# Kernel tuning notes

Measured on AMD Instinct MI355X. Metric: run time of the kernel, lower is better.

## Reference

```python
import jax, jax.numpy as jnp
import numpy as np

# Coefficients of the 16 differentiable logic gates expressed over the basis
# [1, a, b, a*b]. Row i corresponds to gate i in the standard difflogic order:
# 0:0, 1:a&b, 2:a&~b, 3:a, 4:~a&b, 5:b, 6:xor, 7:or, 8:nor, 9:xnor,
# 10:~b, 11:b=>a, 12:~a, 13:a=>b, 14:nand, 15:1
GATE_COEFFS = np.array([
    [0, 0, 0, 0],
    [0, 0, 0, 1],
    [0, 1, 0, -1],
    [0, 1, 0, 0],
    [0, 0, 1, -1],
    [0, 0, 1, 0],
    [0, 1, 1, -2],
    [0, 1, 1, -1],
    [1, -1, -1, 1],
    [1, -1, -1, 2],
    [1, 0, -1, 0],
    [1, 0, -1, 1],
    [1, -1, 0, 0],
    [1, -1, 0, 1],
    [1, 0, 0, -1],
    [1, 0, 0, 0],
], dtype=np.float32)

IN_DIM = 8192
OUT_DIM = 8192
BATCH = 8192
TAU = 1.0


def setup_inputs() -> dict:
    key = jax.random.key(0)
    k1, k2, k3, k4 = jax.random.split(key, 4)
    x = jax.random.uniform(k1, (BATCH, IN_DIM), dtype=jnp.float32)
    weight = jax.random.normal(k2, (OUT_DIM, 16), dtype=jnp.float32)
    idx_a = jax.random.randint(k3, (OUT_DIM,), 0, IN_DIM, dtype=jnp.int64 if jax.config.jax_enable_x64 else jnp.int32)
    idx_b = jax.random.randint(k4, (OUT_DIM,), 0, IN_DIM, dtype=jnp.int64 if jax.config.jax_enable_x64 else jnp.int32)
    return {"x": x, "weight": weight, "idx_a": idx_a, "idx_b": idx_b}


def reference(x, weight, idx_a, idx_b):
    # Gather the two inputs of each neuron: [B, out_dim]
    a = x[:, idx_a]
    b = x[:, idx_b]
    # Soft gate mixture: softmax over 16 gates per neuron (training, 'soft')
    w = jax.nn.softmax(weight / TAU, axis=-1)  # [out_dim, 16]
    # Since every gate is affine in {1, a, b, ab}, collapse the 16-gate
    # weighted sum into per-neuron coefficients: c = w @ G  -> [out_dim, 4]
    c = w @ jnp.asarray(GATE_COEFFS)
    out = c[:, 0] + c[:, 1] * a + c[:, 2] * b + c[:, 3] * (a * b)
    return out
```

## Files before the change

kernel.cpp:

```cpp
#include <hip/hip_runtime.h>
#include <hip/hip_bf16.h>
#include <math.h>

#define IN_DIM  8192
#define OUT_DIM 8192
#define BATCH   8192

__device__ __constant__ float GC0[16] = {0,0,0,0, 0,0,0,0, 1,1,1,1, 1,1,1,1};
__device__ __constant__ float GC1[16] = {0,0,1,1, 0,0,1,1, -1,-1,0,0, -1,-1,0,0};
__device__ __constant__ float GC2[16] = {0,0,0,0, 1,1,1,1, -1,-1,-1,-1, 0,0,0,0};
__device__ __constant__ float GC3[16] = {0,1,-1,0, -1,0,-2,-1, 1,2,0,1, 0,1,-1,0};

__global__ __launch_bounds__(256) void compute_c_kernel(
    const float* __restrict__ weight, float4* __restrict__ c)
{
    int row = blockIdx.x * 256 + threadIdx.x;
    if (row >= OUT_DIM) return;
    const float* wr = weight + (size_t)row * 16;
    float v[16];
    float m = -1e30f;
#pragma unroll
    for (int i = 0; i < 16; ++i) { v[i] = wr[i]; m = fmaxf(m, v[i]); }
    float s = 0.f;
#pragma unroll
    for (int i = 0; i < 16; ++i) { v[i] = __expf(v[i] - m); s += v[i]; }
    float inv = 1.0f / s;
    float c0 = 0.f, c1 = 0.f, c2 = 0.f, c3 = 0.f;
#pragma unroll
    for (int i = 0; i < 16; ++i) {
        c0 = fmaf(v[i], GC0[i], c0);
        c1 = fmaf(v[i], GC1[i], c1);
        c2 = fmaf(v[i], GC2[i], c2);
        c3 = fmaf(v[i], GC3[i], c3);
    }
    c[row] = make_float4(c0 * inv, c1 * inv, c2 * inv, c3 * inv);
}

__global__ __launch_bounds__(256) void gate_main_kernel(
    const float* __restrict__ x,
    const float4* __restrict__ c,
    const int4* __restrict__ ia4,
    const int4* __restrict__ ib4,
    float4* __restrict__ out)
{
    __shared__ float xrow[IN_DIM];
    const int b = blockIdx.x;
    const float4* xr4 = (const float4*)(x + (size_t)b * IN_DIM);
    float4* xs4 = (float4*)xrow;
#pragma unroll
    for (int i = 0; i < IN_DIM / 4 / 256; ++i)
        xs4[i * 256 + threadIdx.x] = xr4[i * 256 + threadIdx.x];
    __syncthreads();

    float4* orow = out + (size_t)b * (OUT_DIM / 4);
#pragma unroll
    for (int it = 0; it < OUT_DIM / 4 / 256; ++it) {
        int j4 = it * 256 + threadIdx.x;
        int4 ia = ia4[j4];
        int4 ib = ib4[j4];
        float4 cA = c[4 * j4 + 0];
        float4 cB = c[4 * j4 + 1];
        float4 cC = c[4 * j4 + 2];
        float4 cD = c[4 * j4 + 3];

        float a0 = xrow[ia.x], b0 = xrow[ib.x];
        float a1 = xrow[ia.y], b1 = xrow[ib.y];
        float a2 = xrow[ia.z], b2 = xrow[ib.z];
        float a3 = xrow[ia.w], b3 = xrow[ib.w];

        float4 o;
        o.x = fmaf(a0, fmaf(b0, cA.w, cA.y), fmaf(b0, cA.z, cA.x));
        o.y = fmaf(a1, fmaf(b1, cB.w, cB.y), fmaf(b1, cB.z, cB.x));
        o.z = fmaf(a2, fmaf(b2, cC.w, cC.y), fmaf(b2, cC.z, cC.x));
        o.w = fmaf(a3, fmaf(b3, cD.w, cD.y), fmaf(b3, cD.z, cD.x));
        orow[j4] = o;
    }
}

extern "C" void kernel_launch(void* const* d_in, const int* in_sizes, int n_in,
                              void* d_out, int out_size, void* d_ws, size_t ws_size,
                              hipStream_t stream) {
    const float* x      = (const float*)d_in[0];
    const float* weight = (const float*)d_in[1];
    const int*   idx_a  = (const int*)d_in[2];
    const int*   idx_b  = (const int*)d_in[3];
    float* out = (float*)d_out;

    float4* c = (float4*)d_ws;

    compute_c_kernel<<<OUT_DIM / 256, 256, 0, stream>>>(weight, c);
    gate_main_kernel<<<BATCH, 256, 0, stream>>>(
        x, c, (const int4*)idx_a, (const int4*)idx_b, (float4*)out);
}
```

Measured before the change: 484.0 us.

## Process two batch rows per block with 1024 threads and nontemporal output stores

```diff
diff --git a/kernel.cpp b/kernel.cpp
--- a/kernel.cpp
+++ b/kernel.cpp
@@ -1,10 +1,13 @@
 #include <hip/hip_runtime.h>
-#include <hip/hip_bf16.h>
 #include <math.h>
 
 #define IN_DIM  8192
 #define OUT_DIM 8192
 #define BATCH   8192
+#define RPB     2
+#define T       1024
+
+typedef float f32x4 __attribute__((ext_vector_type(4)));
 
 __device__ __constant__ float GC0[16] = {0,0,0,0, 0,0,0,0, 1,1,1,1, 1,1,1,1};
 __device__ __constant__ float GC1[16] = {0,0,1,1, 0,0,1,1, -1,-1,0,0, -1,-1,0,0};
@@ -36,26 +39,31 @@
     c[row] = make_float4(c0 * inv, c1 * inv, c2 * inv, c3 * inv);
 }
 
-__global__ __launch_bounds__(256) void gate_main_kernel(
+__global__ __launch_bounds__(T, 8) void gate_main_kernel(
     const float* __restrict__ x,
     const float4* __restrict__ c,
     const int4* __restrict__ ia4,
     const int4* __restrict__ ib4,
-    float4* __restrict__ out)
+    float* __restrict__ out)
 {
-    __shared__ float xrow[IN_DIM];
-    const int b = blockIdx.x;
-    const float4* xr4 = (const float4*)(x + (size_t)b * IN_DIM);
-    float4* xs4 = (float4*)xrow;
+    __shared__ float4 xrow4[RPB * IN_DIM / 4];
+    float* xrow = (float*)xrow4;
+    const size_t b0 = (size_t)blockIdx.x * RPB;
+
+    const float4* xr4 = (const float4*)(x + b0 * IN_DIM);
 #pragma unroll
-    for (int i = 0; i < IN_DIM / 4 / 256; ++i)
-        xs4[i * 256 + threadIdx.x] = xr4[i * 256 + threadIdx.x];
+    for (int i = 0; i < (RPB * IN_DIM / 4) / T; ++i)
+        xrow4[i * T + threadIdx.x] = xr4[i * T + threadIdx.x];
     __syncthreads();
 
-    float4* orow = out + (size_t)b * (OUT_DIM / 4);
+    const float* x0 = xrow;
+    const float* x1 = xrow + IN_DIM;
+    f32x4* orow0 = (f32x4*)(out + b0 * OUT_DIM);
+    f32x4* orow1 = orow0 + (OUT_DIM / 4);
+
 #pragma unroll
-    for (int it = 0; it < OUT_DIM / 4 / 256; ++it) {
-        int j4 = it * 256 + threadIdx.x;
+    for (int it = 0; it < OUT_DIM / 4 / T; ++it) {
+        int j4 = it * T + threadIdx.x;
         int4 ia = ia4[j4];
         int4 ib = ib4[j4];
         float4 cA = c[4 * j4 + 0];
@@ -63,17 +71,30 @@
         float4 cC = c[4 * j4 + 2];
         float4 cD = c[4 * j4 + 3];
 
-        float a0 = xrow[ia.x], b0 = xrow[ib.x];
-        float a1 = xrow[ia.y], b1 = xrow[ib.y];
-        float a2 = xrow[ia.z], b2 = xrow[ib.z];
-        float a3 = xrow[ia.w], b3 = xrow[ib.w];
-
-        float4 o;
-        o.x = fmaf(a0, fmaf(b0, cA.w, cA.y), fmaf(b0, cA.z, cA.x));
-        o.y = fmaf(a1, fmaf(b1, cB.w, cB.y), fmaf(b1, cB.z, cB.x));
-        o.z = fmaf(a2, fmaf(b2, cC.w, cC.y), fmaf(b2, cC.z, cC.x));
-        o.w = fmaf(a3, fmaf(b3, cD.w, cD.y), fmaf(b3, cD.z, cD.x));
-        orow[j4] = o;
+        {
+            float a0 = x0[ia.x], v0 = x0[ib.x];
+            float a1 = x0[ia.y], v1 = x0[ib.y];
+            float a2 = x0[ia.z], v2 = x0[ib.z];
+            float a3 = x0[ia.w], v3 = x0[ib.w];
+            f32x4 o;
+            o.x = fmaf(a0, fmaf(v0, cA.w, cA.y), fmaf(v0, cA.z, cA.x));
+            o.y = fmaf(a1, fmaf(v1, cB.w, cB.y), fmaf(v1, cB.z, cB.x));
+            o.z = fmaf(a2, fmaf(v2, cC.w, cC.y), fmaf(v2, cC.z, cC.x));
+            o.w = fmaf(a3, fmaf(v3, cD.w, cD.y), fmaf(v3, cD.z, cD.x));
+            __builtin_nontemporal_store(o, &orow0[j4]);
+        }
+        {
+            float a0 = x1[ia.x], v0 = x1[ib.x];
+            float a1 = x1[ia.y], v1 = x1[ib.y];
+            float a2 = x1[ia.z], v2 = x1[ib.z];
+            float a3 = x1[ia.w], v3 = x1[ib.w];
+            f32x4 o;
+            o.x = fmaf(a0, fmaf(v0, cA.w, cA.y), fmaf(v0, cA.z, cA.x));
+            o.y = fmaf(a1, fmaf(v1, cB.w, cB.y), fmaf(v1, cB.z, cB.x));
+            o.z = fmaf(a2, fmaf(v2, cC.w, cC.y), fmaf(v2, cC.z, cC.x));
+            o.w = fmaf(a3, fmaf(v3, cD.w, cD.y), fmaf(v3, cD.z, cD.x));
+            __builtin_nontemporal_store(o, &orow1[j4]);
+        }
     }
 }
 
@@ -89,6 +110,6 @@
     float4* c = (float4*)d_ws;
 
     compute_c_kernel<<<OUT_DIM / 256, 256, 0, stream>>>(weight, c);
-    gate_main_kernel<<<BATCH, 256, 0, stream>>>(
-        x, c, (const int4*)idx_a, (const int4*)idx_b, (float4*)out);
+    gate_main_kernel<<<BATCH / RPB, T, 0, stream>>>(
+        x, c, (const int4*)idx_a, (const int4*)idx_b, out);
 }
```

After: 461.5 us. -4.7%, faster.

## Process 16 batch rows per block with register-cached coefficients and double-buffered prefetch

Applied to the files above, without the earlier changes.

```diff
diff --git a/kernel.cpp b/kernel.cpp
--- a/kernel.cpp
+++ b/kernel.cpp
@@ -1,10 +1,11 @@
 #include <hip/hip_runtime.h>
-#include <hip/hip_bf16.h>
 #include <math.h>
 
 #define IN_DIM  8192
 #define OUT_DIM 8192
 #define BATCH   8192
+#define ROWS    16
+#define T       1024
 
 __device__ __constant__ float GC0[16] = {0,0,0,0, 0,0,0,0, 1,1,1,1, 1,1,1,1};
 __device__ __constant__ float GC1[16] = {0,0,1,1, 0,0,1,1, -1,-1,0,0, -1,-1,0,0};
@@ -36,44 +37,74 @@
     c[row] = make_float4(c0 * inv, c1 * inv, c2 * inv, c3 * inv);
 }
 
-__global__ __launch_bounds__(256) void gate_main_kernel(
+__global__ __launch_bounds__(T, 4) void gate_main_kernel(
     const float* __restrict__ x,
     const float4* __restrict__ c,
     const int4* __restrict__ ia4,
     const int4* __restrict__ ib4,
     float4* __restrict__ out)
 {
-    __shared__ float xrow[IN_DIM];
-    const int b = blockIdx.x;
-    const float4* xr4 = (const float4*)(x + (size_t)b * IN_DIM);
-    float4* xs4 = (float4*)xrow;
-#pragma unroll
-    for (int i = 0; i < IN_DIM / 4 / 256; ++i)
-        xs4[i * 256 + threadIdx.x] = xr4[i * 256 + threadIdx.x];
+    __shared__ float buf[2][IN_DIM];
+    const int tid = threadIdx.x;
+    const size_t r0 = (size_t)blockIdx.x * ROWS;
+
+    const int q0 = tid, q1 = tid + T;
+    const int4 iaA = ia4[q0], ibA = ib4[q0];
+    const int4 iaB = ia4[q1], ibB = ib4[q1];
+    const float4 cA0 = c[4*q0+0], cA1 = c[4*q0+1], cA2 = c[4*q0+2], cA3 = c[4*q0+3];
+    const float4 cB0 = c[4*q1+0], cB1 = c[4*q1+1], cB2 = c[4*q1+2], cB3 = c[4*q1+3];
+
+    {
+        const float4* src4 = (const float4*)(x + r0 * IN_DIM);
+        float4* dst4 = (float4*)buf[0];
+        dst4[tid]     = src4[tid];
+        dst4[tid + T] = src4[tid + T];
+    }
     __syncthreads();
 
-    float4* orow = out + (size_t)b * (OUT_DIM / 4);
-#pragma unroll
-    for (int it = 0; it < OUT_DIM / 4 / 256; ++it) {
-        int j4 = it * 256 + threadIdx.x;
-        int4 ia = ia4[j4];
-        int4 ib = ib4[j4];
-        float4 cA = c[4 * j4 + 0];
-        float4 cB = c[4 * j4 + 1];
-        float4 cC = c[4 * j4 + 2];
-        float4 cD = c[4 * j4 + 3];
+    int cur = 0;
+    for (int r = 0; r < ROWS; ++r) {
+        float4 p0 = make_float4(0,0,0,0), p1 = make_float4(0,0,0,0);
+        if (r + 1 < ROWS) {
+            const float4* src4 = (const float4*)(x + (r0 + r + 1) * IN_DIM);
+            p0 = src4[tid];
+            p1 = src4[tid + T];
+        }
 
-        float a0 = xrow[ia.x], b0 = xrow[ib.x];
-        float a1 = xrow[ia.y], b1 = xrow[ib.y];
-        float a2 = xrow[ia.z], b2 = xrow[ib.z];
-        float a3 = xrow[ia.w], b3 = xrow[ib.w];
+        const float* xr = buf[cur];
+        float4* orow = out + (r0 + r) * (OUT_DIM / 4);
+        {
+            float a0 = xr[iaA.x], b0 = xr[ibA.x];
+            float a1 = xr[iaA.y], b1 = xr[ibA.y];
+            float a2 = xr[iaA.z], b2 = xr[ibA.z];
+            float a3 = xr[iaA.w], b3 = xr[ibA.w];
+            float4 o;
+            o.x = fmaf(a0, fmaf(b0, cA0.w, cA0.y), fmaf(b0, cA0.z, cA0.x));
+            o.y = fmaf(a1, fmaf(b1, cA1.w, cA1.y), fmaf(b1, cA1.z, cA1.x));
+            o.z = fmaf(a2, fmaf(b2, cA2.w, cA2.y), fmaf(b2, cA2.z, cA2.x));
+            o.w = fmaf(a3, fmaf(b3, cA3.w, cA3.y), fmaf(b3, cA3.z, cA3.x));
+            orow[q0] = o;
+        }
+        {
+            float a0 = xr[iaB.x], b0 = xr[ibB.x];
+            float a1 = xr[iaB.y], b1 = xr[ibB.y];
+            float a2 = xr[iaB.z], b2 = xr[ibB.z];
+            float a3 = xr[iaB.w], b3 = xr[ibB.w];
+            float4 o;
+            o.x = fmaf(a0, fmaf(b0, cB0.w, cB0.y), fmaf(b0, cB0.z, cB0.x));
+            o.y = fmaf(a1, fmaf(b1, cB1.w, cB1.y), fmaf(b1, cB1.z, cB1.x));
+            o.z = fmaf(a2, fmaf(b2, cB2.w, cB2.y), fmaf(b2, cB2.z, cB2.x));
+            o.w = fmaf(a3, fmaf(b3, cB3.w, cB3.y), fmaf(b3, cB3.z, cB3.x));
+            orow[q1] = o;
+        }
 
-        float4 o;
-        o.x = fmaf(a0, fmaf(b0, cA.w, cA.y), fmaf(b0, cA.z, cA.x));
-        o.y = fmaf(a1, fmaf(b1, cB.w, cB.y), fmaf(b1, cB.z, cB.x));
-        o.z = fmaf(a2, fmaf(b2, cC.w, cC.y), fmaf(b2, cC.z, cC.x));
-        o.w = fmaf(a3, fmaf(b3, cD.w, cD.y), fmaf(b3, cD.z, cD.x));
-        orow[j4] = o;
+        if (r + 1 < ROWS) {
+            float4* dst4 = (float4*)buf[cur ^ 1];
+            dst4[tid]     = p0;
+            dst4[tid + T] = p1;
+        }
+        __syncthreads();
+        cur ^= 1;
     }
 }
 
@@ -89,6 +120,6 @@
     float4* c = (float4*)d_ws;
 
     compute_c_kernel<<<OUT_DIM / 256, 256, 0, stream>>>(weight, c);
-    gate_main_kernel<<<BATCH, 256, 0, stream>>>(
+    gate_main_kernel<<<BATCH / ROWS, T, 0, stream>>>(
         x, c, (const int4*)idx_a, (const int4*)idx_b, (float4*)out);
 }
```

After: 445.9 us. -7.9%, faster.
